# Kernel optimization log

Measured on AMD Instinct MI355X. Metric: run time of the kernel, lower is better.

Reference implementation:

```python
import jax, jax.numpy as jnp
import numpy as np
from jax import lax
from jax.scipy.special import logsumexp

EPS = 0.01 ** 2      # blur^p, geomloss SamplesLoss(p=2, blur=0.01)
N_ITERS = 20         # fixed Sinkhorn iterations (log-domain)


def setup_inputs() -> dict:
    key = jax.random.key(0)
    k1, k2 = jax.random.split(key)
    p_q = jax.random.normal(k1, (4, 4096, 3), dtype=jnp.float32)
    p_gt = jax.random.normal(k2, (4, 4096, 4), dtype=jnp.float32)
    return {"p_q": p_q, "p_gt": p_gt}


def _cost(x, y):
    # C_ij = 0.5 * ||x_i - y_j||^2   (geomloss p=2 convention), [B,N,M]
    x2 = jnp.sum(x * x, -1)
    y2 = jnp.sum(y * y, -1)
    xy = jnp.einsum('bnd,bmd->bnm', x, y)
    return 0.5 * (x2[:, :, None] + y2[:, None, :] - 2.0 * xy)


def _softmin(C, pot, logw, axis):
    # -eps * logsumexp over `axis` of (pot - C)/eps + logw ; pot/logw broadcast on `axis`'s dual
    if axis == 2:
        z = (pot[:, None, :] - C) / EPS + logw  # reduce over M -> [B,N]
    else:
        z = (pot[:, :, None] - C) / EPS + logw  # reduce over N -> [B,M]
    return -EPS * logsumexp(z, axis=axis)


def _ot_potentials(C, loga, logb):
    # asymmetric log-domain Sinkhorn; iterate on detached cost (envelope theorem,
    # matching geomloss' detach-then-extrapolate gradient), final differentiable step.
    Cd = lax.stop_gradient(C)
    B, N, M = C.shape

    def body(i, fg):
        f, g = fg
        f = _softmin(Cd, g, logb, axis=2)
        g = _softmin(Cd, f, loga, axis=1)
        return (f, g)

    f0 = jnp.zeros((B, N), C.dtype)
    g0 = jnp.zeros((B, M), C.dtype)
    f, g = lax.fori_loop(0, N_ITERS, body, (f0, g0))
    fd, gd = lax.stop_gradient(f), lax.stop_gradient(g)
    f = _softmin(C, gd, logb, axis=2)
    g = _softmin(C, fd, loga, axis=1)
    return f, g


def _sym_potential(C, logw):
    # symmetric Sinkhorn for OT(a,a): single potential, damped updates
    Cd = lax.stop_gradient(C)
    B, N, _ = C.shape

    def body(i, f):
        return 0.5 * (f + _softmin(Cd, f, logw, axis=2))

    f = lax.fori_loop(0, N_ITERS, body, jnp.zeros((B, N), C.dtype))
    return _softmin(C, lax.stop_gradient(f), logw, axis=2)


def reference(p_q, p_gt):
    x = p_q                 # [B,N,3]
    y = p_gt[:, :, :3]      # [B,M,3]
    B, N, _ = x.shape
    M = y.shape[1]
    loga = jnp.full((1, 1), -jnp.log(N), x.dtype)  # uniform weights (broadcast)
    logb = jnp.full((1, 1), -jnp.log(M), x.dtype)

    Cxy = _cost(x, y)
    Cxx = _cost(x, x)
    Cyy = _cost(y, y)

    f_ab, g_ab = _ot_potentials(Cxy, loga[:, :, None] * 0 - jnp.log(N), logb)
    # note: loga used in softmin over N-axis needs [.., :, None] broadcast; build explicitly:
    loga_b = jnp.full((B, N, 1), -jnp.log(N), x.dtype)
    logb_b = jnp.full((B, 1, M), -jnp.log(M), x.dtype)
    f_ab = _softmin(Cxy, lax.stop_gradient(g_ab), logb_b, axis=2)  # idempotent re-extrapolation
    g_ab = _softmin(Cxy, lax.stop_gradient(f_ab), loga_b, axis=1)
    f_aa = _sym_potential(Cxx, jnp.full((B, 1, N), -jnp.log(N), x.dtype))
    g_bb = _sym_potential(Cyy, logb_b)

    # debiased Sinkhorn divergence per batch: <a, f_ab - f_aa> + <b, g_ab - g_bb>
    L = jnp.mean(f_ab - f_aa, axis=1) + jnp.mean(g_ab - g_bb, axis=1)
    return L
```

## Files before the change

### kernel.cpp

```cpp
#include <hip/hip_runtime.h>
#include <math.h>

#define NPTS 4096
#define NBATCH 4
#define BLOCK 512
#define RPW 8

static constexpr float KSCALE     = 1.4426950408889634f / 1e-4f;
static constexpr float INVK2      = 1.0f / (KSCALE * KSCALE);
static constexpr float EPSLN2     = 1e-4f * 0.6931471805599453f;
static constexpr float NEGEPSLOGW = 8.31776616671934e-4f;
static constexpr float THR        = 20.0f;

__device__ __forceinline__ float fexp2(float x){
#if __has_builtin(__builtin_amdgcn_exp2f)
  return __builtin_amdgcn_exp2f(x);
#else
  return exp2f(x);
#endif
}
__device__ __forceinline__ float flog2(float x){
#if __has_builtin(__builtin_amdgcn_logf)
  return __builtin_amdgcn_logf(x);
#else
  return log2f(x);
#endif
}
__device__ __forceinline__ float frl(float x){
  return __int_as_float(__builtin_amdgcn_readfirstlane(__float_as_int(x)));
}

__global__ __launch_bounds__(BLOCK, 4) void softmin_kernel(
    const float* __restrict__ rowA, int rsA, const float4* __restrict__ pkInA,
    float4* __restrict__ pkOutA, const float* __restrict__ hOldA,
    float* __restrict__ outA, int modeA,
    const float* __restrict__ rowB, int rsB, const float4* __restrict__ pkInB,
    float4* __restrict__ pkOutB, const float* __restrict__ hOldB,
    float* __restrict__ outB, int modeB)
{
  __shared__ float4 qs[NPTS];

  int bid = blockIdx.x;
  const float* rowp; const float4* pkin; float4* pkout; const float* hold;
  float* outp; int rs, mode;
  if (bid < 256) { rowp=rowA; pkin=pkInA; pkout=pkOutA; hold=hOldA; outp=outA; rs=rsA; mode=modeA; }
  else           { rowp=rowB; pkin=pkInB; pkout=pkOutB; hold=hOldB; outp=outB; rs=rsB; mode=modeB; }
  int lb = bid & 255;
  int b  = lb >> 6;
  int rb = lb & 63;

  int tid = threadIdx.x;
  int lane = tid & 63;
  int wu = __builtin_amdgcn_readfirstlane(tid >> 6);
  int r0 = rb*64 + wu*RPW;
  int ridx0 = b*NPTS + r0;

  {
    const float4* src = pkin + b*NPTS;
    #pragma unroll
    for (int i = 0; i < NPTS/BLOCK; ++i)
      qs[i*BLOCK + tid] = src[i*BLOCK + tid];
  }

  float sx[RPW], sy[RPW], sz[RPW];
  #pragma unroll
  for (int i = 0; i < RPW; ++i) {
    const float* p = rowp + (size_t)(ridx0 + i) * rs;
    sx[i] = frl(p[0]*KSCALE); sy[i] = frl(p[1]*KSCALE); sz[i] = frl(p[2]*KSCALE);
  }

  __syncthreads();

  float cmax[4][RPW];
  #pragma unroll
  for (int c = 0; c < 4; ++c)
    #pragma unroll
    for (int r = 0; r < RPW; ++r) cmax[c][r] = -INFINITY;

  #pragma unroll
  for (int c = 0; c < 4; ++c) {
    #pragma unroll
    for (int g = 0; g < 4; ++g) {
      int base = c*1024 + g*256 + lane;
      float4 q0 = qs[base], q1 = qs[base+64], q2 = qs[base+128], q3 = qs[base+192];
      #pragma unroll
      for (int r = 0; r < RPW; ++r) {
        float t0 = fmaf(sx[r],q0.x,fmaf(sy[r],q0.y,fmaf(sz[r],q0.z,q0.w)));
        float t1 = fmaf(sx[r],q1.x,fmaf(sy[r],q1.y,fmaf(sz[r],q1.z,q1.w)));
        float t2 = fmaf(sx[r],q2.x,fmaf(sy[r],q2.y,fmaf(sz[r],q2.z,q2.w)));
        float t3 = fmaf(sx[r],q3.x,fmaf(sy[r],q3.y,fmaf(sz[r],q3.z,q3.w)));
        float u  = fmaxf(fmaxf(t0,t1),t2);
        cmax[c][r] = fmaxf(fmaxf(u,t3),cmax[c][r]);
      }
    }
  }

  float M[RPW];
  #pragma unroll
  for (int r = 0; r < RPW; ++r) {
    float mm = fmaxf(fmaxf(cmax[0][r],cmax[1][r]), fmaxf(cmax[2][r],cmax[3][r]));
    #pragma unroll
    for (int off = 32; off; off >>= 1) mm = fmaxf(mm, __shfl_xor(mm, off, 64));
    M[r] = mm;
  }

  float S[RPW];
  #pragma unroll
  for (int r = 0; r < RPW; ++r) S[r] = 0.f;

  #pragma unroll
  for (int c = 0; c < 4; ++c) {
    int am = 0;
    #pragma unroll
    for (int r = 0; r < RPW; ++r)
      am |= __any(cmax[c][r] > M[r] - THR) ? (1 << r) : 0;
    if (am) {
      #pragma unroll
      for (int g = 0; g < 4; ++g) {
        int base = c*1024 + g*256 + lane;
        float4 q0 = qs[base], q1 = qs[base+64], q2 = qs[base+128], q3 = qs[base+192];
        #pragma unroll
        for (int r = 0; r < RPW; ++r) if (am & (1 << r)) {
          float t0 = fmaf(sx[r],q0.x,fmaf(sy[r],q0.y,fmaf(sz[r],q0.z,q0.w)));
          float t1 = fmaf(sx[r],q1.x,fmaf(sy[r],q1.y,fmaf(sz[r],q1.z,q1.w)));
          float t2 = fmaf(sx[r],q2.x,fmaf(sy[r],q2.y,fmaf(sz[r],q2.z,q2.w)));
          float t3 = fmaf(sx[r],q3.x,fmaf(sy[r],q3.y,fmaf(sz[r],q3.z,q3.w)));
          float e0 = fexp2(t0-M[r]) + fexp2(t1-M[r]);
          float e1 = fexp2(t2-M[r]) + fexp2(t3-M[r]);
          S[r] += e0 + e1;
        }
      }
    }
  }

  #pragma unroll
  for (int r = 0; r < RPW; ++r) {
    float s = S[r];
    #pragma unroll
    for (int off = 32; off; off >>= 1) s += __shfl_xor(s, off, 64);
    float ch = 0.5f*(sx[r]*sx[r] + sy[r]*sy[r] + sz[r]*sz[r]) * INVK2;
    float res = fmaf(-EPSLN2, M[r] + flog2(s), ch + NEGEPSLOGW);
    if (lane == r) {
      if (mode) res = 0.5f*(hold[ridx0 + r] + res);
      outp[ridx0 + r] = res;
      ((float*)(pkout + (ridx0 + r)))[3] = (res - ch) * KSCALE;
    }
  }
}

__global__ void pack_init(const float* __restrict__ x, const float* __restrict__ y,
                          float4* pkfab, float4* pkgab,
                          float4* pkfaa0, float4* pkfaa1,
                          float4* pkgbb0, float4* pkgbb1)
{
  int i = blockIdx.x*256 + threadIdx.x;
  const float* xp = x + (size_t)i*3;
  float xx = xp[0], xy = xp[1], xz = xp[2];
  float4 vx; vx.x=xx; vx.y=xy; vx.z=xz;
  vx.w = -0.5f*(xx*xx + xy*xy + xz*xz)*KSCALE;
  const float* yp = y + (size_t)i*4;
  float yx = yp[0], yy = yp[1], yz = yp[2];
  float4 vy; vy.x=yx; vy.y=yy; vy.z=yz;
  vy.w = -0.5f*(yx*yx + yy*yy + yz*yz)*KSCALE;
  pkgab[i]  = vx; pkfaa0[i] = vx; pkfaa1[i] = vx;
  pkfab[i]  = vy; pkgbb0[i] = vy; pkgbb1[i] = vy;
}

__global__ void reduce_kernel(const float* __restrict__ fab, const float* __restrict__ faa,
                              const float* __restrict__ gab, const float* __restrict__ gbb,
                              float* __restrict__ out)
{
  int b = blockIdx.x;
  int tid = threadIdx.x;
  float s = 0.f;
  for (int i = tid; i < NPTS; i += 256) {
    int idx = b*NPTS + i;
    s += (fab[idx] - faa[idx]) + (gab[idx] - gbb[idx]);
  }
  for (int off = 32; off > 0; off >>= 1) s += __shfl_down(s, off, 64);
  __shared__ float red[4];
  if ((tid & 63) == 0) red[tid >> 6] = s;
  __syncthreads();
  if (tid == 0) out[b] = (red[0]+red[1]+red[2]+red[3]) * (1.0f/NPTS);
}

extern "C" void kernel_launch(void* const* d_in, const int* in_sizes, int n_in,
                              void* d_out, int out_size, void* d_ws, size_t ws_size,
                              hipStream_t stream)
{
  const float* x = (const float*)d_in[0];
  const float* y = (const float*)d_in[1];
  float* ws = (float*)d_ws;
  const size_t P = (size_t)NBATCH * NPTS;

  float* f_ab    = ws + 0*P;
  float* g_ab    = ws + 1*P;
  float* faaR[2] = { ws + 2*P, ws + 4*P };
  float* gbbR[2] = { ws + 3*P, ws + 5*P };
  float4* pk4    = (float4*)(ws + 6*P);
  float4* PKfab    = pk4 + 0*P;
  float4* PKgab    = pk4 + 1*P;
  float4* PKfaa[2] = { pk4 + 2*P, pk4 + 3*P };
  float4* PKgbb[2] = { pk4 + 4*P, pk4 + 5*P };

  hipMemsetAsync(ws + 2*P, 0, 2*P*sizeof(float), stream);
  pack_init<<<dim3(P/256), dim3(256), 0, stream>>>(x, y, PKfab, PKgab,
                                                   PKfaa[0], PKfaa[1], PKgbb[0], PKgbb[1]);

  for (int i = 0; i < 21; ++i) {
    int cur = i & 1, nxt = cur ^ 1;
    int modeS = (i < 20) ? 1 : 0;
    softmin_kernel<<<512, BLOCK, 0, stream>>>(
        x, 3, PKfab, PKgab, f_ab, f_ab, 0,
        x, 3, PKfaa[cur], PKfaa[nxt], faaR[cur], faaR[nxt], modeS);
    softmin_kernel<<<512, BLOCK, 0, stream>>>(
        y, 4, PKgab, PKfab, g_ab, g_ab, 0,
        y, 4, PKgbb[cur], PKgbb[nxt], gbbR[cur], gbbR[nxt], modeS);
  }
  reduce_kernel<<<dim3(4), dim3(256), 0, stream>>>(f_ab, faaR[1], g_ab, gbbR[1], (float*)d_out);
}
```

Measured before the change: 1.016 ms.

## Repack point data into paired SoA layout and use packed v2f FMAs

```diff
diff --git a/kernel.cpp b/kernel.cpp
--- a/kernel.cpp
+++ b/kernel.cpp
@@ -3,8 +3,11 @@
 
 #define NPTS 4096
 #define NBATCH 4
+#define NPAIR 2048
 #define BLOCK 512
 #define RPW 8
+
+typedef float v2f __attribute__((ext_vector_type(2)));
 
 static constexpr float KSCALE     = 1.4426950408889634f / 1e-4f;
 static constexpr float INVK2      = 1.0f / (KSCALE * KSCALE);
@@ -28,6 +31,9 @@
 }
 __device__ __forceinline__ float frl(float x){
   return __int_as_float(__builtin_amdgcn_readfirstlane(__float_as_int(x)));
+}
+__device__ __forceinline__ v2f fma2(float s, v2f b, v2f c){
+  return __builtin_elementwise_fma((v2f){s,s}, b, c);
 }
 
 __global__ __launch_bounds__(BLOCK, 4) void softmin_kernel(
@@ -38,7 +44,8 @@
     float4* __restrict__ pkOutB, const float* __restrict__ hOldB,
     float* __restrict__ outB, int modeB)
 {
-  __shared__ float4 qs[NPTS];
+  __shared__ float4 qsA[NPAIR];
+  __shared__ float4 qsB[NPAIR];
 
   int bid = blockIdx.x;
   const float* rowp; const float4* pkin; float4* pkout; const float* hold;
@@ -56,10 +63,13 @@
   int ridx0 = b*NPTS + r0;
 
   {
-    const float4* src = pkin + b*NPTS;
-    #pragma unroll
-    for (int i = 0; i < NPTS/BLOCK; ++i)
-      qs[i*BLOCK + tid] = src[i*BLOCK + tid];
+    const float4* srcA = pkin + (size_t)b*NPAIR;
+    const float4* srcB = pkin + 4*NPAIR + (size_t)b*NPAIR;
+    #pragma unroll
+    for (int i = 0; i < NPAIR/BLOCK; ++i) {
+      qsA[i*BLOCK + tid] = srcA[i*BLOCK + tid];
+      qsB[i*BLOCK + tid] = srcB[i*BLOCK + tid];
+    }
   }
 
   float sx[RPW], sy[RPW], sz[RPW];
@@ -81,16 +91,17 @@
   for (int c = 0; c < 4; ++c) {
     #pragma unroll
     for (int g = 0; g < 4; ++g) {
-      int base = c*1024 + g*256 + lane;
-      float4 q0 = qs[base], q1 = qs[base+64], q2 = qs[base+128], q3 = qs[base+192];
+      int base = c*512 + g*128 + lane;
+      float4 A0 = qsA[base], A1 = qsA[base+64];
+      float4 B0 = qsB[base], B1 = qsB[base+64];
+      v2f x0 = {A0.x,A0.y}, y0 = {A0.z,A0.w}, z0 = {B0.x,B0.y}, w0 = {B0.z,B0.w};
+      v2f x1 = {A1.x,A1.y}, y1 = {A1.z,A1.w}, z1 = {B1.x,B1.y}, w1 = {B1.z,B1.w};
       #pragma unroll
       for (int r = 0; r < RPW; ++r) {
-        float t0 = fmaf(sx[r],q0.x,fmaf(sy[r],q0.y,fmaf(sz[r],q0.z,q0.w)));
-        float t1 = fmaf(sx[r],q1.x,fmaf(sy[r],q1.y,fmaf(sz[r],q1.z,q1.w)));
-        float t2 = fmaf(sx[r],q2.x,fmaf(sy[r],q2.y,fmaf(sz[r],q2.z,q2.w)));
-        float t3 = fmaf(sx[r],q3.x,fmaf(sy[r],q3.y,fmaf(sz[r],q3.z,q3.w)));
-        float u  = fmaxf(fmaxf(t0,t1),t2);
-        cmax[c][r] = fmaxf(fmaxf(u,t3),cmax[c][r]);
+        v2f t0 = fma2(sx[r], x0, fma2(sy[r], y0, fma2(sz[r], z0, w0)));
+        v2f t1 = fma2(sx[r], x1, fma2(sy[r], y1, fma2(sz[r], z1, w1)));
+        v2f m2 = __builtin_elementwise_max(t0, t1);
+        cmax[c][r] = fmaxf(fmaxf(m2.x, m2.y), cmax[c][r]);
       }
     }
   }
@@ -117,17 +128,22 @@
     if (am) {
       #pragma unroll
       for (int g = 0; g < 4; ++g) {
-        int base = c*1024 + g*256 + lane;
-        float4 q0 = qs[base], q1 = qs[base+64], q2 = qs[base+128], q3 = qs[base+192];
+        int base = c*512 + g*128 + lane;
+        float4 A0 = qsA[base], A1 = qsA[base+64];
+        float4 B0 = qsB[base], B1 = qsB[base+64];
+        v2f x0 = {A0.x,A0.y}, y0 = {A0.z,A0.w}, z0 = {B0.x,B0.y}, w0 = {B0.z,B0.w};
+        v2f x1 = {A1.x,A1.y}, y1 = {A1.z,A1.w}, z1 = {B1.x,B1.y}, w1 = {B1.z,B1.w};
         #pragma unroll
         for (int r = 0; r < RPW; ++r) if (am & (1 << r)) {
-          float t0 = fmaf(sx[r],q0.x,fmaf(sy[r],q0.y,fmaf(sz[r],q0.z,q0.w)));
-          float t1 = fmaf(sx[r],q1.x,fmaf(sy[r],q1.y,fmaf(sz[r],q1.z,q1.w)));
-          float t2 = fmaf(sx[r],q2.x,fmaf(sy[r],q2.y,fmaf(sz[r],q2.z,q2.w)));
-          float t3 = fmaf(sx[r],q3.x,fmaf(sy[r],q3.y,fmaf(sz[r],q3.z,q3.w)));
-          float e0 = fexp2(t0-M[r]) + fexp2(t1-M[r]);
-          float e1 = fexp2(t2-M[r]) + fexp2(t3-M[r]);
-          S[r] += e0 + e1;
+          v2f t0 = fma2(sx[r], x0, fma2(sy[r], y0, fma2(sz[r], z0, w0)));
+          v2f t1 = fma2(sx[r], x1, fma2(sy[r], y1, fma2(sz[r], z1, w1)));
+          v2f m2 = __builtin_elementwise_max(t0, t1);
+          float gm = fmaxf(m2.x, m2.y);
+          if (__any(gm > M[r] - THR)) {
+            float e0 = fexp2(t0.x-M[r]) + fexp2(t0.y-M[r]);
+            float e1 = fexp2(t1.x-M[r]) + fexp2(t1.y-M[r]);
+            S[r] += e0 + e1;
+          }
         }
       }
     }
@@ -143,7 +159,9 @@
     if (lane == r) {
       if (mode) res = 0.5f*(hold[ridx0 + r] + res);
       outp[ridx0 + r] = res;
-      ((float*)(pkout + (ridx0 + r)))[3] = (res - ch) * KSCALE;
+      int row = r0 + r;
+      float* pw = (float*)(pkout + 4*NPAIR + (size_t)b*NPAIR + (row >> 1));
+      pw[2 + (row & 1)] = (res - ch) * KSCALE;
     }
   }
 }
@@ -154,16 +172,25 @@
                           float4* pkgbb0, float4* pkgbb1)
 {
   int i = blockIdx.x*256 + threadIdx.x;
+  int b = i >> 12, j = i & 4095;
+  int p = j >> 1, s = j & 1;
+  size_t aOff = ((size_t)b*NPAIR + p)*4;
+  size_t bOff = ((size_t)4*NPAIR + (size_t)b*NPAIR + p)*4;
+
   const float* xp = x + (size_t)i*3;
   float xx = xp[0], xy = xp[1], xz = xp[2];
-  float4 vx; vx.x=xx; vx.y=xy; vx.z=xz;
-  vx.w = -0.5f*(xx*xx + xy*xy + xz*xz)*KSCALE;
+  float xw = -0.5f*(xx*xx + xy*xy + xz*xz)*KSCALE;
   const float* yp = y + (size_t)i*4;
   float yx = yp[0], yy = yp[1], yz = yp[2];
-  float4 vy; vy.x=yx; vy.y=yy; vy.z=yz;
-  vy.w = -0.5f*(yx*yx + yy*yy + yz*yz)*KSCALE;
-  pkgab[i]  = vx; pkfaa0[i] = vx; pkfaa1[i] = vx;
-  pkfab[i]  = vy; pkgbb0[i] = vy; pkgbb1[i] = vy;
+  float yw = -0.5f*(yx*yx + yy*yy + yz*yz)*KSCALE;
+
+  float* f;
+  f = (float*)pkgab;  f[aOff+s]=xx; f[aOff+2+s]=xy; f[bOff+s]=xz; f[bOff+2+s]=xw;
+  f = (float*)pkfaa0; f[aOff+s]=xx; f[aOff+2+s]=xy; f[bOff+s]=xz; f[bOff+2+s]=xw;
+  f = (float*)pkfaa1; f[aOff+s]=xx; f[aOff+2+s]=xy; f[bOff+s]=xz; f[bOff+2+s]=xw;
+  f = (float*)pkfab;  f[aOff+s]=yx; f[aOff+2+s]=yy; f[bOff+s]=yz; f[bOff+2+s]=yw;
+  f = (float*)pkgbb0; f[aOff+s]=yx; f[aOff+2+s]=yy; f[bOff+s]=yz; f[bOff+2+s]=yw;
+  f = (float*)pkgbb1; f[aOff+s]=yx; f[aOff+2+s]=yy; f[bOff+s]=yz; f[bOff+2+s]=yw;
 }
 
 __global__ void reduce_kernel(const float* __restrict__ fab, const float* __restrict__ faa,
```

Result: slower. 1.390 ms (+36.8%).
